# Optimization experiments

Hardware: AMD Instinct MI355X
Metric: run time of the kernel (lower is better)

The kernel has to match this reference:

```python
import jax, jax.numpy as jnp
import numpy as np
from functools import partial

B = 256          # batch_size (== hidden_dim, required by the module's broadcasting)
T = 512          # seq_length
H = 256          # hidden_dim == dim_out
E = 6            # emb_dim
V = 10           # num_input_digits
C = 10           # num_classes


def _kaiming(key, shape):
    fan_in = shape[1]
    return jax.random.normal(key, shape, dtype=jnp.float32) * np.sqrt(2.0 / fan_in)


def setup_inputs() -> dict:
    key = jax.random.key(0)
    ks = jax.random.split(key, 12)
    inp = {
        "x": jax.random.randint(ks[0], (B, T), 0, V),
        "emb": jax.random.normal(ks[1], (V, E), dtype=jnp.float32),
        "Wxg": _kaiming(ks[2], (H, E)), "Whg": _kaiming(ks[3], (H, H)), "bg": jnp.zeros((H,), jnp.float32),
        "Wxi": _kaiming(ks[4], (H, E)), "Whi": _kaiming(ks[5], (H, H)), "bi": jnp.zeros((H,), jnp.float32),
        "Wxf": _kaiming(ks[6], (H, E)), "Whf": _kaiming(ks[7], (H, H)), "bf": jnp.zeros((H,), jnp.float32),
        "Wxo": _kaiming(ks[8], (H, E)), "Who": _kaiming(ks[9], (H, H)), "bo": jnp.zeros((H,), jnp.float32),
        "Wp": _kaiming(ks[10], (C, H)), "bp": jnp.zeros((C,), jnp.float32),
    }
    return inp


def reference(x, emb, Wxg, Whg, bg, Wxi, Whi, bi, Wxf, Whf, bf, Wxo, Who, bo, Wp, bp):
    # x: (B, T) int -> embed -> (B, T, E)
    xe = emb[x]
    # time-major (T, E, B): each step uses x_t.T as in the torch code
    xt_seq = jnp.transpose(xe, (1, 2, 0))

    h0 = jnp.zeros((H, B), jnp.float32)  # h lives as (H, B) per original math
    c0 = jnp.zeros((H, B), jnp.float32)

    def step(carry, xTt):  # xTt: (E, B)
        h, c = carry
        # NOTE: bias (H,) broadcasts over the trailing batch axis (H==B), faithful
        # to the original torch broadcasting.
        g = jnp.tanh(Wxg @ xTt + Whg @ h + bg)
        i = jax.nn.sigmoid(Wxi @ xTt + Whi @ h + bi)
        f = jax.nn.sigmoid(Wxf @ xTt + Whf @ h + bf)
        o = jax.nn.sigmoid(Wxo @ xTt + Who @ h + bo)
        c = g * i + c * f
        h = jnp.tanh(c) * o
        return (h, c), None

    (h, c), _ = jax.lax.scan(step, (h0, c0), xt_seq)
    return (Wp @ h).T + bp  # (B, C)
```

## Files before the change

kernel.cpp:

```cpp
#include <hip/hip_runtime.h>
#include <hip/hip_bf16.h>


typedef __attribute__((ext_vector_type(4))) int   int4v;
typedef __attribute__((ext_vector_type(4))) float float4v;

#define MFMA_I8(a, b, c) __builtin_amdgcn_mfma_i32_16x16x64_i8(a, b, c, 0, 0, 0)

#define K_TANH (-2.8853900817779268f)
#define K_SIG  (-1.4426950408889634f)

#define HSTRIDE 320

__device__ __forceinline__ short f2b(float f) {
    __hip_bfloat16 b = __float2bfloat16(f); return *(short*)&b;
}
__device__ __forceinline__ float b2f(short s) {
    union { unsigned int u; float f; } v; v.u = ((unsigned int)(unsigned short)s) << 16; return v.f;
}
__device__ __forceinline__ float fexp2(float x) {
#if __has_builtin(__builtin_amdgcn_exp2f)
    return __builtin_amdgcn_exp2f(x);
#else
    return __expf(x * 0.6931471805599453f);
#endif
}
__device__ __forceinline__ float frcp(float x) { return __builtin_amdgcn_rcpf(x); }
__device__ __forceinline__ float clamp60(float x) { return __builtin_amdgcn_fmed3f(x, -60.f, 60.f); }

__global__ __attribute__((amdgpu_flat_work_group_size(512, 512), amdgpu_waves_per_eu(2, 2)))
void lstm_i8(
    const int* __restrict__ x,
    const float* __restrict__ emb,
    const float* __restrict__ Wxg, const float* __restrict__ Whg, const float* __restrict__ bg,
    const float* __restrict__ Wxi, const float* __restrict__ Whi, const float* __restrict__ bi,
    const float* __restrict__ Wxf, const float* __restrict__ Whf, const float* __restrict__ bff,
    const float* __restrict__ Wxo, const float* __restrict__ Who, const float* __restrict__ bo,
    const float* __restrict__ Wp, const float* __restrict__ bp,
    float* __restrict__ out)
{
    const int tid = threadIdx.x, bid = blockIdx.x;
    const int c0 = bid * 2;
    const int w = tid >> 6, lane = tid & 63;
    const int l = lane & 15, q = lane >> 4;
    const int col = l & 1;
    const int g3  = (l >> 1) & 7;
    const int si  = g3 & 3;
    const int srr = g3 >> 2;
    const int rw  = 32 * w;
    const int row = rw + 16 * srr + 4 * q + si;

    __shared__ __align__(16) unsigned int hbuf[2][2 * HSTRIDE / 4];
    __shared__ __align__(16) short hfin[2 * 264];
    __shared__ unsigned char xdig2[512 * 2];
    __shared__ __align__(16) float tblT[10 * 1024];
    __shared__ float scaleL[4 * 256];

    const float* WxT[4] = {Wxg, Wxi, Wxf, Wxo};
    const float* WhT[4] = {Whg, Whi, Whf, Who};

    if (tid < 2 * HSTRIDE / 4) hbuf[0][tid] = 0u;
    for (int i = tid; i < 1024; i += 512)
        xdig2[i] = (unsigned char)x[(c0 + (i & 1)) * 512 + (i >> 1)];

    for (int i = tid; i < 2560; i += 512) {
        int d = i >> 8, r = i & 255;
        float4v v;
        #pragma unroll
        for (int g = 0; g < 4; g++) {
            float s = 0.f;
            #pragma unroll
            for (int e = 0; e < 6; e++) s += WxT[g][r * 6 + e] * emb[d * 6 + e];
            v[g] = s * (g == 0 ? K_TANH : K_SIG);
        }
        *(float4v*)&tblT[d * 1024 + r * 4] = v;
    }

    int4v wa[4][2][4];
    #pragma unroll
    for (int g = 0; g < 4; g++)
        #pragma unroll
        for (int rr = 0; rr < 2; rr++) {
            const float* Wr = WhT[g] + (rw + 16 * rr + l) * 256 + q * 16;
            float mx = 0.f;
            #pragma unroll
            for (int kt = 0; kt < 4; kt++)
                #pragma unroll
                for (int c4 = 0; c4 < 4; c4++) {
                    float4v v = *(const float4v*)(Wr + kt * 64 + c4 * 4);
                    #pragma unroll
                    for (int j = 0; j < 4; j++) mx = fmaxf(mx, fabsf(v[j]));
                }
            mx = fmaxf(mx, __shfl_xor(mx, 16));
            mx = fmaxf(mx, __shfl_xor(mx, 32));
            mx = fmaxf(mx, 1e-20f);
            if (q == 0) scaleL[g * 256 + rw + 16 * rr + l] = mx;
            float qs = 127.f / mx;
            #pragma unroll
            for (int kt = 0; kt < 4; kt++) {
                int4v f;
                #pragma unroll
                for (int dw = 0; dw < 4; dw++) {
                    float4v v = *(const float4v*)(Wr + kt * 64 + dw * 4);
                    int word = 0;
                    #pragma unroll
                    for (int byt = 0; byt < 4; byt++) {
                        int z = (int)rintf(v[byt] * qs);
                        word |= (z & 255) << (8 * byt);
                    }
                    f[dw] = word;
                }
                wa[g][rr][kt] = f;
            }
        }

    __syncthreads();

    float dscl[4];
    #pragma unroll
    for (int g = 0; g < 4; g++) {
        float kk = (g == 0 ? K_TANH : K_SIG) * (1.f / 16129.f);
        dscl[g] = scaleL[g * 256 + row] * kk;
    }
    float bSc[4];
    bSc[0] = bg[c0 + col] * K_TANH; bSc[1] = bi[c0 + col] * K_SIG;
    bSc[2] = bff[c0 + col] * K_SIG; bSc[3] = bo[c0 + col] * K_SIG;

    const bool bi1 = (si & 1) != 0;
    const bool bi2 = (si & 2) != 0;
    const bool brr = (srr != 0);
    const float* tprow = tblT + row * 4;
    const int hoff = col * HSTRIDE + rw + 16 * srr + 4 * q;

    float cs = 0.f, hl = 0.f;

    for (int t = 0; t < 512; t++) {
        const int p = t & 1;
        const char* hbase = (const char*)hbuf[p] + col * HSTRIDE + q * 16;

        int4v acc[4][2];
        #pragma unroll
        for (int g = 0; g < 4; g++)
            #pragma unroll
            for (int rr = 0; rr < 2; rr++)
                acc[g][rr] = (int4v){0, 0, 0, 0};

        int dg = xdig2[t * 2 + col];
        float4v tb = *(const float4v*)(tprow + dg * 1024);

        #pragma unroll
        for (int kt = 0; kt < 4; kt++) {
            int4v hf = *(const int4v*)(hbase + kt * 64);
            #pragma unroll
            for (int g = 0; g < 4; g++) {
                acc[g][0] = MFMA_I8(wa[g][0][kt], hf, acc[g][0]);
                acc[g][1] = MFMA_I8(wa[g][1][kt], hf, acc[g][1]);
            }
        }

        int av[4];
        #pragma unroll
        for (int g = 0; g < 4; g++) {
            int s00 = bi1 ? acc[g][0][1] : acc[g][0][0];
            int s01 = bi1 ? acc[g][0][3] : acc[g][0][2];
            int s10 = bi1 ? acc[g][1][1] : acc[g][1][0];
            int s11 = bi1 ? acc[g][1][3] : acc[g][1][2];
            int s0  = bi2 ? s01 : s00;
            int s1  = bi2 ? s11 : s10;
            av[g]   = brr ? s1 : s0;
        }
        {
            float pg = clamp60(fmaf((float)av[0], dscl[0], tb[0] + bSc[0]));
            float pi = clamp60(fmaf((float)av[1], dscl[1], tb[1] + bSc[1]));
            float pf = clamp60(fmaf((float)av[2], dscl[2], tb[2] + bSc[2]));
            float po = clamp60(fmaf((float)av[3], dscl[3], tb[3] + bSc[3]));
            float Eg = fexp2(pg), Ei = fexp2(pi), Ef = fexp2(pf), Eo = fexp2(po);
            float t1 = (1.f - Eg) * frcp((1.f + Eg) * (1.f + Ei));
            float c  = fmaf(cs, frcp(1.f + Ef), t1);
            cs = c;
            float Ec = fexp2(clamp60(K_TANH * c));
            float hh = (1.f - Ec) * frcp((1.f + Ec) * (1.f + Eo));
            hl = hh;
            int hq = (int)rintf(hh * 127.f) & 255;
            int w1 = hq | (__shfl_xor(hq, 2) << 8);
            int w2 = w1 | (__shfl_xor(w1, 4) << 16);
            if (si == 0)
                *(int*)((char*)hbuf[1 - p] + hoff) = w2;
        }
        __syncthreads();
    }

    hfin[col * 264 + row] = f2b(hl);
    __syncthreads();

    if (tid < 20) {
        int pc = tid / 10, cls = tid - pc * 10;
        const short* hcol = &hfin[pc * 264];
        const float* wrow = Wp + cls * 256;
        float s = 0.f;
        #pragma unroll 8
        for (int k = 0; k < 256; k++) s += b2f(hcol[k]) * wrow[k];
        out[(c0 + pc) * 10 + cls] = s + bp[cls];
    }
}

extern "C" void kernel_launch(void* const* d_in, const int* in_sizes, int n_in,
                              void* d_out, int out_size, void* d_ws, size_t ws_size,
                              hipStream_t stream) {
    const int*   x   = (const int*)d_in[0];
    const float* emb = (const float*)d_in[1];
    const float* Wxg = (const float*)d_in[2];
    const float* Whg = (const float*)d_in[3];
    const float* bg  = (const float*)d_in[4];
    const float* Wxi = (const float*)d_in[5];
    const float* Whi = (const float*)d_in[6];
    const float* bi  = (const float*)d_in[7];
    const float* Wxf = (const float*)d_in[8];
    const float* Whf = (const float*)d_in[9];
    const float* bff = (const float*)d_in[10];
    const float* Wxo = (const float*)d_in[11];
    const float* Who = (const float*)d_in[12];
    const float* bo  = (const float*)d_in[13];
    const float* Wp  = (const float*)d_in[14];
    const float* bp  = (const float*)d_in[15];

    hipLaunchKernelGGL(lstm_i8, dim3(128), dim3(512), 0, stream,
                       x, emb, Wxg, Whg, bg, Wxi, Whi, bi, Wxf, Whf, bff,
                       Wxo, Who, bo, Wp, bp, (float*)d_out);
}
```

Measured before the change: 635.2 us.

## Double block to 1024 threads, one row tile per wave, byte h stores

Each block now runs 16 waves instead of 8, and each wave owns a 16-row tile instead of 32 rows. This halves the MFMA chain and the register footprint per wave at every serial timestep. The shuffle-based packing of quantized h into words is replaced by single-byte LDS stores, and the exp-argument clamps are removed. The risks are a costlier 1024-thread barrier on every one of the 512 steps and possible inf/NaN handling differences without the clamp.

```diff
diff --git a/kernel.cpp b/kernel.cpp
--- a/kernel.cpp
+++ b/kernel.cpp
@@ -26,9 +26,8 @@
 #endif
 }
 __device__ __forceinline__ float frcp(float x) { return __builtin_amdgcn_rcpf(x); }
-__device__ __forceinline__ float clamp60(float x) { return __builtin_amdgcn_fmed3f(x, -60.f, 60.f); }
-
-__global__ __attribute__((amdgpu_flat_work_group_size(512, 512), amdgpu_waves_per_eu(2, 2)))
+
+__global__ __attribute__((amdgpu_flat_work_group_size(1024, 1024), amdgpu_waves_per_eu(4, 4)))
 void lstm_i8(
     const int* __restrict__ x,
     const float* __restrict__ emb,
@@ -44,11 +43,10 @@
     const int w = tid >> 6, lane = tid & 63;
     const int l = lane & 15, q = lane >> 4;
     const int col = l & 1;
-    const int g3  = (l >> 1) & 7;
-    const int si  = g3 & 3;
-    const int srr = g3 >> 2;
-    const int rw  = 32 * w;
-    const int row = rw + 16 * srr + 4 * q + si;
+    const int si  = (l >> 1) & 3;
+    const int dup = (l >> 3) & 1;
+    const int rw  = 16 * w;
+    const int row = rw + 4 * q + si;
 
     __shared__ __align__(16) unsigned int hbuf[2][2 * HSTRIDE / 4];
     __shared__ __align__(16) short hfin[2 * 264];
@@ -60,10 +58,10 @@
     const float* WhT[4] = {Whg, Whi, Whf, Who};
 
     if (tid < 2 * HSTRIDE / 4) hbuf[0][tid] = 0u;
-    for (int i = tid; i < 1024; i += 512)
-        xdig2[i] = (unsigned char)x[(c0 + (i & 1)) * 512 + (i >> 1)];
-
-    for (int i = tid; i < 2560; i += 512) {
+    if (tid < 1024)
+        xdig2[tid] = (unsigned char)x[(c0 + (tid & 1)) * 512 + (tid >> 1)];
+
+    for (int i = tid; i < 2560; i += 1024) {
         int d = i >> 8, r = i & 255;
         float4v v;
         #pragma unroll
@@ -76,43 +74,41 @@
         *(float4v*)&tblT[d * 1024 + r * 4] = v;
     }
 
-    int4v wa[4][2][4];
+    int4v wa[4][4];
     #pragma unroll
-    for (int g = 0; g < 4; g++)
-        #pragma unroll
-        for (int rr = 0; rr < 2; rr++) {
-            const float* Wr = WhT[g] + (rw + 16 * rr + l) * 256 + q * 16;
-            float mx = 0.f;
-            #pragma unroll
-            for (int kt = 0; kt < 4; kt++)
+    for (int g = 0; g < 4; g++) {
+        const float* Wr = WhT[g] + (rw + l) * 256 + q * 16;
+        float mx = 0.f;
+        #pragma unroll
+        for (int kt = 0; kt < 4; kt++)
+            #pragma unroll
+            for (int c4 = 0; c4 < 4; c4++) {
+                float4v v = *(const float4v*)(Wr + kt * 64 + c4 * 4);
                 #pragma unroll
-                for (int c4 = 0; c4 < 4; c4++) {
-                    float4v v = *(const float4v*)(Wr + kt * 64 + c4 * 4);
-                    #pragma unroll
-                    for (int j = 0; j < 4; j++) mx = fmaxf(mx, fabsf(v[j]));
+                for (int j = 0; j < 4; j++) mx = fmaxf(mx, fabsf(v[j]));
+            }
+        mx = fmaxf(mx, __shfl_xor(mx, 16));
+        mx = fmaxf(mx, __shfl_xor(mx, 32));
+        mx = fmaxf(mx, 1e-20f);
+        if (q == 0) scaleL[g * 256 + rw + l] = mx;
+        float qs = 127.f / mx;
+        #pragma unroll
+        for (int kt = 0; kt < 4; kt++) {
+            int4v f;
+            #pragma unroll
+            for (int dw = 0; dw < 4; dw++) {
+                float4v v = *(const float4v*)(Wr + kt * 64 + dw * 4);
+                int word = 0;
+                #pragma unroll
+                for (int byt = 0; byt < 4; byt++) {
+                    int z = (int)rintf(v[byt] * qs);
+                    word |= (z & 255) << (8 * byt);
                 }
-            mx = fmaxf(mx, __shfl_xor(mx, 16));
-            mx = fmaxf(mx, __shfl_xor(mx, 32));
-            mx = fmaxf(mx, 1e-20f);
-            if (q == 0) scaleL[g * 256 + rw + 16 * rr + l] = mx;
-            float qs = 127.f / mx;
-            #pragma unroll
-            for (int kt = 0; kt < 4; kt++) {
-                int4v f;
-                #pragma unroll
-                for (int dw = 0; dw < 4; dw++) {
-                    float4v v = *(const float4v*)(Wr + kt * 64 + dw * 4);
-                    int word = 0;
-                    #pragma unroll
-                    for (int byt = 0; byt < 4; byt++) {
-                        int z = (int)rintf(v[byt] * qs);
-                        word |= (z & 255) << (8 * byt);
-                    }
-                    f[dw] = word;
-                }
-                wa[g][rr][kt] = f;
+                f[dw] = word;
             }
-        }
+            wa[g][kt] = f;
+        }
+    }
 
     __syncthreads();
 
@@ -128,9 +124,8 @@
 
     const bool bi1 = (si & 1) != 0;
     const bool bi2 = (si & 2) != 0;
-    const bool brr = (srr != 0);
     const float* tprow = tblT + row * 4;
-    const int hoff = col * HSTRIDE + rw + 16 * srr + 4 * q;
+    const int hoff = col * HSTRIDE + row;
 
     float cs = 0.f, hl = 0.f;
 
@@ -138,12 +133,9 @@
         const int p = t & 1;
         const char* hbase = (const char*)hbuf[p] + col * HSTRIDE + q * 16;
 
-        int4v acc[4][2];
-        #pragma unroll
-        for (int g = 0; g < 4; g++)
-            #pragma unroll
-            for (int rr = 0; rr < 2; rr++)
-                acc[g][rr] = (int4v){0, 0, 0, 0};
+        int4v acc[4];
+        #pragma unroll
+        for (int g = 0; g < 4; g++) acc[g] = (int4v){0, 0, 0, 0};
 
         int dg = xdig2[t * 2 + col];
         float4v tb = *(const float4v*)(tprow + dg * 1024);
@@ -152,45 +144,36 @@
         for (int kt = 0; kt < 4; kt++) {
             int4v hf = *(const int4v*)(hbase + kt * 64);
             #pragma unroll
-            for (int g = 0; g < 4; g++) {
-                acc[g][0] = MFMA_I8(wa[g][0][kt], hf, acc[g][0]);
-                acc[g][1] = MFMA_I8(wa[g][1][kt], hf, acc[g][1]);
-            }
+            for (int g = 0; g < 4; g++)
+                acc[g] = MFMA_I8(wa[g][kt], hf, acc[g]);
         }
 
         int av[4];
         #pragma unroll
         for (int g = 0; g < 4; g++) {
-            int s00 = bi1 ? acc[g][0][1] : acc[g][0][0];
-            int s01 = bi1 ? acc[g][0][3] : acc[g][0][2];
-            int s10 = bi1 ? acc[g][1][1] : acc[g][1][0];
-            int s11 = bi1 ? acc[g][1][3] : acc[g][1][2];
-            int s0  = bi2 ? s01 : s00;
-            int s1  = bi2 ? s11 : s10;
-            av[g]   = brr ? s1 : s0;
+            int s0 = bi1 ? acc[g][1] : acc[g][0];
+            int s1 = bi1 ? acc[g][3] : acc[g][2];
+            av[g]  = bi2 ? s1 : s0;
         }
         {
-            float pg = clamp60(fmaf((float)av[0], dscl[0], tb[0] + bSc[0]));
-            float pi = clamp60(fmaf((float)av[1], dscl[1], tb[1] + bSc[1]));
-            float pf = clamp60(fmaf((float)av[2], dscl[2], tb[2] + bSc[2]));
-            float po = clamp60(fmaf((float)av[3], dscl[3], tb[3] + bSc[3]));
+            float pg = fmaf((float)av[0], dscl[0], tb[0] + bSc[0]);
+            float pi = fmaf((float)av[1], dscl[1], tb[1] + bSc[1]);
+            float pf = fmaf((float)av[2], dscl[2], tb[2] + bSc[2]);
+            float po = fmaf((float)av[3], dscl[3], tb[3] + bSc[3]);
             float Eg = fexp2(pg), Ei = fexp2(pi), Ef = fexp2(pf), Eo = fexp2(po);
             float t1 = (1.f - Eg) * frcp((1.f + Eg) * (1.f + Ei));
             float c  = fmaf(cs, frcp(1.f + Ef), t1);
             cs = c;
-            float Ec = fexp2(clamp60(K_TANH * c));
+            float Ec = fexp2(K_TANH * c);
             float hh = (1.f - Ec) * frcp((1.f + Ec) * (1.f + Eo));
             hl = hh;
-            int hq = (int)rintf(hh * 127.f) & 255;
-            int w1 = hq | (__shfl_xor(hq, 2) << 8);
-            int w2 = w1 | (__shfl_xor(w1, 4) << 16);
-            if (si == 0)
-                *(int*)((char*)hbuf[1 - p] + hoff) = w2;
+            if (dup == 0)
+                *((char*)hbuf[1 - p] + hoff) = (char)((int)rintf(hh * 127.f));
         }
         __syncthreads();
     }
 
-    hfin[col * 264 + row] = f2b(hl);
+    if (dup == 0) hfin[col * 264 + row] = f2b(hl);
     __syncthreads();
 
     if (tid < 20) {
@@ -224,7 +207,7 @@
     const float* Wp  = (const float*)d_in[14];
     const float* bp  = (const float*)d_in[15];
 
-    hipLaunchKernelGGL(lstm_i8, dim3(128), dim3(512), 0, stream,
+    hipLaunchKernelGGL(lstm_i8, dim3(128), dim3(1024), 0, stream,
                        x, emb, Wxg, Whg, bg, Wxi, Whi, bi, Wxf, Whf, bff,
                        Wxo, Who, bo, Wp, bp, (float*)d_out);
 }
```

Measured after the change: 573.6 us. -9.7%, faster.
